# Optimization experiments

Measured on AMD Instinct MI355X. Metric: run time of the kernel, lower is better.

Reference implementation:

```python
import jax, jax.numpy as jnp
import numpy as np
import math

D_MODEL, N_HEADS, D_K, D_V = 512, 2, 64, 64
C_CLIP = 10.0
MASK_FILL = -10.0

def setup_inputs() -> dict:
    key = jax.random.key(0)
    ks = jax.random.split(key, 12)
    B, Lq, Lk = 4, 2048, 2048
    s = 1.0 / math.sqrt(D_MODEL)
    return {
        "Q": jax.random.normal(ks[0], (B, Lq, D_MODEL), jnp.float32),
        "K": jax.random.normal(ks[1], (B, Lk, D_MODEL), jnp.float32),
        "V": jax.random.normal(ks[2], (B, Lk, D_MODEL), jnp.float32),
        "mask": jax.random.randint(ks[3], (B, Lk), 0, 2) > 0,
        "Wq": jax.random.normal(ks[4], (D_MODEL, N_HEADS * D_K), jnp.float32) * s,
        "bq": jnp.zeros((N_HEADS * D_K,), jnp.float32),
        "Wk": jax.random.normal(ks[5], (D_MODEL, N_HEADS * D_K), jnp.float32) * s,
        "bk": jnp.zeros((N_HEADS * D_K,), jnp.float32),
        "Wv": jax.random.normal(ks[6], (D_MODEL, N_HEADS * D_V), jnp.float32) * s,
        "bv": jnp.zeros((N_HEADS * D_V,), jnp.float32),
        "Wo": jax.random.normal(ks[7], (N_HEADS * D_V, D_MODEL), jnp.float32) * s,
        "bo": jnp.zeros((D_MODEL,), jnp.float32),
    }

def reference(Q, K, V, mask, Wq, bq, Wk, bk, Wv, bv, Wo, bo):
    B, Lq, _ = Q.shape
    Lk = K.shape[1]
    # project and split heads: [B, h, L, d]
    q = (Q @ Wq + bq).reshape(B, Lq, N_HEADS, D_K).transpose(0, 2, 1, 3)
    k = (K @ Wk + bk).reshape(B, Lk, N_HEADS, D_K).transpose(0, 2, 1, 3)
    v = (V @ Wv + bv).reshape(B, Lk, N_HEADS, D_V).transpose(0, 2, 1, 3)
    scores = jnp.einsum("bhqd,bhkd->bhqk", q, k) / jnp.sqrt(jnp.float32(D_K))
    scores = jnp.tanh(scores) * C_CLIP
    scores = jnp.where(mask[:, None, None, :], MASK_FILL, scores)
    attn = jax.nn.log_softmax(scores, axis=-1)  # NOTE: log-softmax used directly as weights
    out = jnp.einsum("bhqk,bhkd->bhqd", attn, v)
    out = out.transpose(0, 2, 1, 3).reshape(B, Lq, N_HEADS * D_V)
    out = out @ Wo + bo
    return (out, attn)
```

## Files before the change

kernel.cpp:

```cpp
#include <hip/hip_runtime.h>

typedef __attribute__((ext_vector_type(8))) short short8;
typedef __attribute__((ext_vector_type(4))) float f32x4;

#define DEVI static __device__ __forceinline__

constexpr int NB   = 4;
constexpr int NH   = 2;
constexpr int SEQ  = 2048;
constexpr int DM   = 512;
constexpr int DKV  = 64;
constexpr int HDIM = 128;

DEVI unsigned short f2bf(float f) {
    union { float f; unsigned u; } v; v.f = f;
    unsigned r = v.u + 0x7FFFu + ((v.u >> 16) & 1u);
    return (unsigned short)(r >> 16);
}
DEVI float bf2f(unsigned short s) {
    union { unsigned u; float f; } v; v.u = ((unsigned)s) << 16; return v.f;
}
DEVI void async16(const void* g, void* l) {
    __builtin_amdgcn_global_load_lds(
        (const __attribute__((address_space(1))) unsigned int*)g,
        (__attribute__((address_space(3))) unsigned int*)l, 16, 0, 0);
}

__global__ __launch_bounds__(256) void k_prep(
    const float* __restrict__ Wq, const float* __restrict__ Wk,
    const float* __restrict__ Wv, const float* __restrict__ Wo,
    unsigned short* __restrict__ Wqt, unsigned short* __restrict__ Wkt,
    unsigned short* __restrict__ Wvt, unsigned short* __restrict__ Wot) {
    int id = blockIdx.x * 256 + threadIdx.x;
    int which = id >> 16;
    int rem = id & 65535;
    if (which < 3) {
        const float* W = which == 0 ? Wq : (which == 1 ? Wk : Wv);
        unsigned short* Wt = which == 0 ? Wqt : (which == 1 ? Wkt : Wvt);
        int n = rem >> 9, k = rem & 511;
        Wt[rem] = f2bf(W[k * HDIM + n]);
    } else {
        int n = rem >> 7, k = rem & 127;
        Wot[rem] = f2bf(Wo[k * DM + n]);
    }
}

__global__ __launch_bounds__(256) void k_proj(
    const float* __restrict__ Qg, const float* __restrict__ Kg, const float* __restrict__ Vg,
    const unsigned short* __restrict__ Wqt, const unsigned short* __restrict__ Wkt,
    const unsigned short* __restrict__ Wvt,
    const float* __restrict__ bq, const float* __restrict__ bk, const float* __restrict__ bv,
    unsigned short* __restrict__ qs, unsigned short* __restrict__ kb,
    unsigned short* __restrict__ vt) {
    __shared__ unsigned short lA[32 * 64];
    __shared__ unsigned short lB[128 * 64];

    const int y = blockIdx.y;
    const float* X = y == 0 ? Qg : (y == 1 ? Kg : Vg);
    const unsigned short* Wt = y == 0 ? Wqt : (y == 1 ? Wkt : Wvt);
    const float* bias = y == 0 ? bq : (y == 1 ? bk : bv);
    const float scal = y == 0 ? 0.25f : 1.0f;
    const int row0 = blockIdx.x * 32;
    const int tid = threadIdx.x, lane = tid & 63, wv = tid >> 6;
    const int l16 = lane & 15, lq4 = lane >> 4;
    const int wc = wv;

    f32x4 acc[2][2];
    #pragma unroll
    for (int i = 0; i < 2; ++i)
        #pragma unroll
        for (int j = 0; j < 2; ++j) acc[i][j] = f32x4{0.f, 0.f, 0.f, 0.f};

    const int arow = tid >> 3, ac0 = (tid & 7) * 8;

    for (int kc = 0; kc < 8; ++kc) {
        {
            const float* src = X + (size_t)(row0 + arow) * DM + kc * 64 + ac0;
            float4 v0 = *(const float4*)src;
            float4 v1 = *(const float4*)(src + 4);
            unsigned q0 = (unsigned)f2bf(v0.x) | ((unsigned)f2bf(v0.y) << 16);
            unsigned q1 = (unsigned)f2bf(v0.z) | ((unsigned)f2bf(v0.w) << 16);
            unsigned q2 = (unsigned)f2bf(v1.x) | ((unsigned)f2bf(v1.y) << 16);
            unsigned q3 = (unsigned)f2bf(v1.z) | ((unsigned)f2bf(v1.w) << 16);
            int slot = (tid & 7) ^ (arow & 7);
            unsigned* d = (unsigned*)((char*)lA + arow * 128 + slot * 16);
            d[0] = q0; d[1] = q1; d[2] = q2; d[3] = q3;
        }
        #pragma unroll
        for (int c = 0; c < 4; ++c) {
            int chunk = wv * 4 + c;
            int n = chunk * 8 + (lane >> 3);
            int gslot = (lane & 7) ^ (n & 7);
            const void* g = (const char*)Wt + ((size_t)n * DM + kc * 64) * 2 + gslot * 16;
            void* l = (char*)lB + chunk * 1024 + lane * 16;
            async16(g, l);
        }
        __syncthreads();

        #pragma unroll
        for (int ks = 0; ks < 2; ++ks) {
            short8 a[2], b[2];
            #pragma unroll
            for (int mt = 0; mt < 2; ++mt) {
                int m = mt * 16 + l16;
                unsigned ao = (unsigned)(m * 128 + ks * 64 + lq4 * 16) ^ ((unsigned)(m & 7) << 4);
                a[mt] = *(const short8*)((const char*)lA + ao);
            }
            #pragma unroll
            for (int nt = 0; nt < 2; ++nt) {
                int n = wc * 32 + nt * 16 + l16;
                unsigned bo2 = (unsigned)(n * 128 + ks * 64 + lq4 * 16) ^ ((unsigned)(n & 7) << 4);
                b[nt] = *(const short8*)((const char*)lB + bo2);
            }
            #pragma unroll
            for (int mt = 0; mt < 2; ++mt)
                #pragma unroll
                for (int nt = 0; nt < 2; ++nt)
                    acc[mt][nt] = __builtin_amdgcn_mfma_f32_16x16x32_bf16(
                        a[mt], b[nt], acc[mt][nt], 0, 0, 0);
        }
        __syncthreads();
    }

    if (y < 2) {
        unsigned short* dstp = (y == 0) ? qs : kb;
        #pragma unroll
        for (int mt = 0; mt < 2; ++mt)
            #pragma unroll
            for (int nt = 0; nt < 2; ++nt) {
                int col = wc * 32 + nt * 16 + l16;
                float bb = bias[col];
                int h = col >> 6, d = col & 63;
                #pragma unroll
                for (int r = 0; r < 4; ++r) {
                    int row = row0 + mt * 16 + lq4 * 4 + r;
                    int b = row >> 11, pos = row & 2047;
                    float val = (acc[mt][nt][r] + bb) * scal;
                    dstp[((size_t)(b * NH + h) * SEQ + pos) * DKV + d] = f2bf(val);
                }
            }
    } else {
        #pragma unroll
        for (int mt = 0; mt < 2; ++mt)
            #pragma unroll
            for (int nt = 0; nt < 2; ++nt) {
                int col = wc * 32 + nt * 16 + l16;
                float bb = bias[col];
                #pragma unroll
                for (int r = 0; r < 4; ++r) {
                    int mrow = mt * 16 + lq4 * 4 + r;
                    lB[col * 32 + mrow] = f2bf(acc[mt][nt][r] + bb);
                }
            }
        __syncthreads();
        int c = tid >> 1, mp = (tid & 1) * 16;
        int b = row0 >> 11, kpos0 = row0 & 2047;
        int h = c >> 6, d = c & 63;
        unsigned short* dst = vt + ((size_t)(b * NH + h) * DKV + d) * SEQ + kpos0 + mp;
        const unsigned short* srcl = &lB[c * 32 + mp];
        *(uint4*)dst = *(const uint4*)srcl;
        *(uint4*)(dst + 8) = *(const uint4*)(srcl + 8);
    }
}

__global__ __launch_bounds__(512) void k_vsum(const unsigned short* __restrict__ vt,
                                              float* __restrict__ vs) {
    int bh = blockIdx.x, tid = threadIdx.x;
    int d = tid >> 3, oct = tid & 7;
    const unsigned short* src = vt + ((size_t)bh * DKV + d) * SEQ + oct * 256;
    float s = 0.f;
    #pragma unroll 4
    for (int i = 0; i < 32; ++i) {
        short8 v = *(const short8*)(src + i * 8);
        #pragma unroll
        for (int t = 0; t < 8; ++t) s += bf2f((unsigned short)v[t]);
    }
    s += __shfl_xor(s, 1); s += __shfl_xor(s, 2); s += __shfl_xor(s, 4);
    if (oct == 0) vs[bh * DKV + d] = s;
}

__global__ __launch_bounds__(1024, 4) void k_fused(
    const unsigned short* __restrict__ qs, const unsigned short* __restrict__ kb,
    const unsigned short* __restrict__ vt, const int* __restrict__ maskg,
    const float* __restrict__ vsumG, float* __restrict__ attnG,
    unsigned short* __restrict__ outh) {
    __shared__ unsigned short sAttn[32 * 2048];
    __shared__ float lsum[8][32];
    __shared__ float lL[32];
    __shared__ float pvbuf[8][16][16];

    const int wg = blockIdx.x;
    const int swz = (wg & 7) * 64 + (wg >> 3);
    const int bh = swz >> 6;
    const int qt = swz & 63;
    const int qbase = qt * 32;
    const int b = bh >> 1, h = bh & 1;
    const int tid = threadIdx.x, lane = tid & 63, wv = tid >> 6;
    const int l16 = lane & 15, lq4 = lane >> 4;
    const int wr = wv >> 3, wc8 = wv & 7;

    const unsigned short* qrow =
        qs + ((size_t)bh * SEQ + qbase + wr * 16 + l16) * DKV + lq4 * 8;
    short8 aq0 = *(const short8*)qrow;
    short8 aq1 = *(const short8*)(qrow + 32);

    const unsigned short* kfrag =
        kb + ((size_t)bh * SEQ + wc8 * 16 + l16) * DKV + lq4 * 8;
    const int* mrow = maskg + b * SEQ + wc8 * 16 + l16;

    const int srow = wr * 16 + lq4 * 4;
    const int cb = wc8 * 16 + l16;

    float sums[4] = {0.f, 0.f, 0.f, 0.f};

    short8 b0 = *(const short8*)kfrag;
    short8 b1 = *(const short8*)(kfrag + 32);
    int mv = mrow[0];
    for (int kt = 0; kt < 16; ++kt) {
        int nx = (kt + 1) & 15;
        short8 nb0 = *(const short8*)(kfrag + (size_t)nx * 8192);
        short8 nb1 = *(const short8*)(kfrag + (size_t)nx * 8192 + 32);
        int nmv = mrow[nx * 128];
        f32x4 acc = f32x4{0.f, 0.f, 0.f, 0.f};
        acc = __builtin_amdgcn_mfma_f32_16x16x32_bf16(aq0, b0, acc, 0, 0, 0);
        acc = __builtin_amdgcn_mfma_f32_16x16x32_bf16(aq1, b1, acc, 0, 0, 0);
        int col = kt * 128 + cb;
        #pragma unroll
        for (int r = 0; r < 4; ++r) {
            float x = acc[r];
            float e2 = __expf(x);
            float s10 = 10.f - 20.f * __builtin_amdgcn_rcpf(1.f + e2);
            float s = mv ? -10.f : s10;
            sums[r] += __expf(s);
            int row = srow + r;
            unsigned bo = (unsigned)(row * 4096 + col * 2) ^ ((unsigned)(row & 7) << 4);
            *(unsigned short*)((char*)sAttn + bo) = f2bf(s);
        }
        b0 = nb0; b1 = nb1; mv = nmv;
    }

    #pragma unroll
    for (int r = 0; r < 4; ++r) {
        float v = sums[r];
        v += __shfl_xor(v, 1); v += __shfl_xor(v, 2);
        v += __shfl_xor(v, 4); v += __shfl_xor(v, 8);
        if (l16 == 0) lsum[wc8][srow + r] = v;
    }
    __syncthreads();
    if (tid < 32) {
        float t = lsum[0][tid] + lsum[1][tid] + lsum[2][tid] + lsum[3][tid] +
                  lsum[4][tid] + lsum[5][tid] + lsum[6][tid] + lsum[7][tid];
        lL[tid] = __logf(t);
    }
    __syncthreads();

    {
        const int row = tid >> 5;
        const int cb2 = (tid & 31) * 8;
        const float Lv = lL[row];
        float* gdst = attnG + ((size_t)bh * SEQ + qbase + row) * SEQ;
        const unsigned rbase = (unsigned)(row * 4096);
        const unsigned rxor = (unsigned)(row & 7) << 4;
        #pragma unroll
        for (int j = 0; j < 8; ++j) {
            int c = cb2 + j * 256;
            unsigned bo = (rbase + (unsigned)(c * 2)) ^ rxor;
            short8 v = *(const short8*)((const char*)sAttn + bo);
            float4 fa, fb;
            fa.x = bf2f((unsigned short)v[0]) - Lv;
            fa.y = bf2f((unsigned short)v[1]) - Lv;
            fa.z = bf2f((unsigned short)v[2]) - Lv;
            fa.w = bf2f((unsigned short)v[3]) - Lv;
            fb.x = bf2f((unsigned short)v[4]) - Lv;
            fb.y = bf2f((unsigned short)v[5]) - Lv;
            fb.z = bf2f((unsigned short)v[6]) - Lv;
            fb.w = bf2f((unsigned short)v[7]) - Lv;
            *(float4*)(gdst + c) = fa;
            *(float4*)(gdst + c + 4) = fb;
        }
    }

    const int kh = wv >> 3, dg = (wv >> 1) & 3, pr = wv & 1;
    const unsigned short* vfrag =
        vt + ((size_t)bh * DKV + dg * 16 + l16) * SEQ + kh * 1024 + lq4 * 8;
    const int arow = pr * 16 + l16;
    const unsigned abase = (unsigned)(arow * 4096 + kh * 2048 + lq4 * 16);
    const unsigned axor = (unsigned)(arow & 7) << 4;
    f32x4 o = f32x4{0.f, 0.f, 0.f, 0.f};
    short8 vf = *(const short8*)vfrag;
    for (int ks = 0; ks < 32; ++ks) {
        short8 nvf = *(const short8*)(vfrag + ((ks + 1) & 31) * 32);
        short8 af = *(const short8*)((const char*)sAttn +
                                     ((abase + (unsigned)(ks * 64)) ^ axor));
        o = __builtin_amdgcn_mfma_f32_16x16x32_bf16(af, vf, o, 0, 0, 0);
        vf = nvf;
    }
    if (kh) {
        #pragma unroll
        for (int r = 0; r < 4; ++r) pvbuf[dg * 2 + pr][lq4 * 4 + r][l16] = o[r];
    }
    __syncthreads();
    if (!kh) {
        const float vs = vsumG[bh * DKV + dg * 16 + l16];
        #pragma unroll
        for (int r = 0; r < 4; ++r) {
            int qr = pr * 16 + lq4 * 4 + r;
            float val = o[r] + pvbuf[dg * 2 + pr][lq4 * 4 + r][l16] - lL[qr] * vs;
            outh[((size_t)b * SEQ + qbase + qr) * HDIM + h * DKV + dg * 16 + l16] =
                f2bf(val);
        }
    }
}

__global__ __launch_bounds__(256) void k_oproj(
    const unsigned short* __restrict__ outh, const unsigned short* __restrict__ Wot,
    const float* __restrict__ bo, float* __restrict__ outG) {
    __shared__ unsigned short lA2[128 * 128];
    __shared__ unsigned short lB2[128 * 128];
    const int row0 = blockIdx.x * 128, col0 = blockIdx.y * 128;
    const int tid = threadIdx.x, lane = tid & 63, wv = tid >> 6;
    const int l16 = lane & 15, lq4 = lane >> 4;
    const int wr = wv >> 1, wc = wv & 1;

    #pragma unroll
    for (int c = 0; c < 8; ++c) {
        int chunk = wv * 8 + c;
        int row = chunk * 4 + (lane >> 4);
        int gslot = (lane & 15) ^ (row & 7);
        async16((const char*)outh + ((size_t)(row0 + row)) * 256 + gslot * 16,
                (char*)lA2 + chunk * 1024 + lane * 16);
    }
    #pragma unroll
    for (int c = 0; c < 8; ++c) {
        int chunk = wv * 8 + c;
        int row = chunk * 4 + (lane >> 4);
        int gslot = (lane & 15) ^ (row & 7);
        async16((const char*)Wot + ((size_t)(col0 + row)) * 256 + gslot * 16,
                (char*)lB2 + chunk * 1024 + lane * 16);
    }
    __syncthreads();

    f32x4 acc[4][4];
    #pragma unroll
    for (int mt = 0; mt < 4; ++mt)
        #pragma unroll
        for (int nt = 0; nt < 4; ++nt) acc[mt][nt] = f32x4{0.f, 0.f, 0.f, 0.f};

    #pragma unroll
    for (int ks = 0; ks < 4; ++ks) {
        short8 a[4], bfr[4];
        #pragma unroll
        for (int mt = 0; mt < 4; ++mt) {
            int m = wr * 64 + mt * 16 + l16;
            unsigned ao = (unsigned)(m * 256 + ks * 64 + lq4 * 16) ^ ((unsigned)(m & 7) << 4);
            a[mt] = *(const short8*)((const char*)lA2 + ao);
        }
        #pragma unroll
        for (int nt = 0; nt < 4; ++nt) {
            int n = wc * 64 + nt * 16 + l16;
            unsigned bo2 = (unsigned)(n * 256 + ks * 64 + lq4 * 16) ^ ((unsigned)(n & 7) << 4);
            bfr[nt] = *(const short8*)((const char*)lB2 + bo2);
        }
        #pragma unroll
        for (int mt = 0; mt < 4; ++mt)
            #pragma unroll
            for (int nt = 0; nt < 4; ++nt)
                acc[mt][nt] = __builtin_amdgcn_mfma_f32_16x16x32_bf16(
                    a[mt], bfr[nt], acc[mt][nt], 0, 0, 0);
    }

    #pragma unroll
    for (int nt = 0; nt < 4; ++nt) {
        int col = col0 + wc * 64 + nt * 16 + l16;
        float bb = bo[col];
        #pragma unroll
        for (int mt = 0; mt < 4; ++mt)
            #pragma unroll
            for (int r = 0; r < 4; ++r) {
                int row = row0 + wr * 64 + mt * 16 + lq4 * 4 + r;
                outG[(size_t)row * DM + col] = acc[mt][nt][r] + bb;
            }
    }
}

extern "C" void kernel_launch(void* const* d_in, const int* in_sizes, int n_in,
                              void* d_out, int out_size, void* d_ws, size_t ws_size,
                              hipStream_t stream) {
    (void)in_sizes; (void)n_in; (void)out_size; (void)ws_size;
    const float* Qg = (const float*)d_in[0];
    const float* Kg = (const float*)d_in[1];
    const float* Vg = (const float*)d_in[2];
    const int*   maskg = (const int*)d_in[3];
    const float* Wq = (const float*)d_in[4];
    const float* bq = (const float*)d_in[5];
    const float* Wk = (const float*)d_in[6];
    const float* bk = (const float*)d_in[7];
    const float* Wv = (const float*)d_in[8];
    const float* bv = (const float*)d_in[9];
    const float* Wo = (const float*)d_in[10];
    const float* bo = (const float*)d_in[11];

    char* ws = (char*)d_ws;
    unsigned short* qs   = (unsigned short*)(ws);
    unsigned short* kb   = (unsigned short*)(ws + (4  << 20));
    unsigned short* vt   = (unsigned short*)(ws + (8  << 20));
    unsigned short* outh = (unsigned short*)(ws + (28 << 20));
    float*          vsum = (float*)(ws + (30 << 20));
    unsigned short* Wqt  = (unsigned short*)(ws + (30 << 20) + 262144);
    unsigned short* Wkt  = (unsigned short*)((char*)Wqt + 131072);
    unsigned short* Wvt  = (unsigned short*)((char*)Wkt + 131072);
    unsigned short* Wot  = (unsigned short*)((char*)Wvt + 131072);

    float* outG  = (float*)d_out;
    float* attnG = outG + (size_t)NB * SEQ * DM;

    hipLaunchKernelGGL(k_prep, dim3(1024), dim3(256), 0, stream,
                       Wq, Wk, Wv, Wo, Wqt, Wkt, Wvt, Wot);
    hipLaunchKernelGGL(k_proj, dim3(256, 3), dim3(256), 0, stream,
                       Qg, Kg, Vg, Wqt, Wkt, Wvt, bq, bk, bv, qs, kb, vt);
    hipLaunchKernelGGL(k_vsum, dim3(8), dim3(512), 0, stream, vt, vsum);
    hipLaunchKernelGGL(k_fused, dim3(512), dim3(1024), 0, stream,
                       qs, kb, vt, maskg, vsum, attnG, outh);
    hipLaunchKernelGGL(k_oproj, dim3(64, 4), dim3(256), 0, stream, outh, Wot, bo, outG);
}
```

Measured before the change: 283.7 us.

## Split fused attention into QK and PV kernels; double-buffer projection GEMM

The fused attention kernel, which held a 32x2048 score tile in LDS, is split into two kernels. k_qk computes clipped, masked scores for 16-row tiles, writes bf16 scores and the per-row log-sum-exp to a global workspace. k_pvfin then reads them back to compute the PV product and write the fp32 log-softmax output. Separately, the projection GEMM gets double-buffered LDS with register prefetch of the next X chunk, overlapping loads with MFMA. The split aims to cut LDS use and raise occupancy, at the cost of a 64MB bf16 score round-trip through global memory.

```diff
diff --git a/kernel.cpp b/kernel.cpp
--- a/kernel.cpp
+++ b/kernel.cpp
@@ -19,6 +19,9 @@
 }
 DEVI float bf2f(unsigned short s) {
     union { unsigned u; float f; } v; v.u = ((unsigned)s) << 16; return v.f;
+}
+DEVI unsigned pk2(float a, float b) {
+    return (unsigned)f2bf(a) | ((unsigned)f2bf(b) << 16);
 }
 DEVI void async16(const void* g, void* l) {
     __builtin_amdgcn_global_load_lds(
@@ -52,8 +55,8 @@
     const float* __restrict__ bq, const float* __restrict__ bk, const float* __restrict__ bv,
     unsigned short* __restrict__ qs, unsigned short* __restrict__ kb,
     unsigned short* __restrict__ vt) {
-    __shared__ unsigned short lA[32 * 64];
-    __shared__ unsigned short lB[128 * 64];
+    __shared__ unsigned short lA[2][32 * 64];
+    __shared__ unsigned short lB[2][128 * 64];
 
     const int y = blockIdx.y;
     const float* X = y == 0 ? Qg : (y == 1 ? Kg : Vg);
@@ -72,31 +75,42 @@
         for (int j = 0; j < 2; ++j) acc[i][j] = f32x4{0.f, 0.f, 0.f, 0.f};
 
     const int arow = tid >> 3, ac0 = (tid & 7) * 8;
-
-    for (int kc = 0; kc < 8; ++kc) {
-        {
-            const float* src = X + (size_t)(row0 + arow) * DM + kc * 64 + ac0;
-            float4 v0 = *(const float4*)src;
-            float4 v1 = *(const float4*)(src + 4);
-            unsigned q0 = (unsigned)f2bf(v0.x) | ((unsigned)f2bf(v0.y) << 16);
-            unsigned q1 = (unsigned)f2bf(v0.z) | ((unsigned)f2bf(v0.w) << 16);
-            unsigned q2 = (unsigned)f2bf(v1.x) | ((unsigned)f2bf(v1.y) << 16);
-            unsigned q3 = (unsigned)f2bf(v1.z) | ((unsigned)f2bf(v1.w) << 16);
-            int slot = (tid & 7) ^ (arow & 7);
-            unsigned* d = (unsigned*)((char*)lA + arow * 128 + slot * 16);
-            d[0] = q0; d[1] = q1; d[2] = q2; d[3] = q3;
-        }
+    const int aslot = (tid & 7) ^ (arow & 7);
+    const float* xsrc = X + (size_t)(row0 + arow) * DM + ac0;
+
+    float4 x0 = *(const float4*)xsrc;
+    float4 x1 = *(const float4*)(xsrc + 4);
+    {
         #pragma unroll
         for (int c = 0; c < 4; ++c) {
             int chunk = wv * 4 + c;
             int n = chunk * 8 + (lane >> 3);
             int gslot = (lane & 7) ^ (n & 7);
-            const void* g = (const char*)Wt + ((size_t)n * DM + kc * 64) * 2 + gslot * 16;
-            void* l = (char*)lB + chunk * 1024 + lane * 16;
-            async16(g, l);
-        }
-        __syncthreads();
-
+            async16((const char*)Wt + ((size_t)n * DM) * 2 + gslot * 16,
+                    (char*)lB[0] + chunk * 1024 + lane * 16);
+        }
+    }
+    float4 y0 = *(const float4*)(xsrc + 64);
+    float4 y1 = *(const float4*)(xsrc + 68);
+    {
+        unsigned* d = (unsigned*)((char*)lA[0] + arow * 128 + aslot * 16);
+        d[0] = pk2(x0.x, x0.y); d[1] = pk2(x0.z, x0.w);
+        d[2] = pk2(x1.x, x1.y); d[3] = pk2(x1.z, x1.w);
+    }
+    __syncthreads();
+
+    for (int kc = 0; kc < 8; ++kc) {
+        const int cur = kc & 1, nxt = cur ^ 1;
+        if (kc < 7) {
+            #pragma unroll
+            for (int c = 0; c < 4; ++c) {
+                int chunk = wv * 4 + c;
+                int n = chunk * 8 + (lane >> 3);
+                int gslot = (lane & 7) ^ (n & 7);
+                async16((const char*)Wt + ((size_t)n * DM + (kc + 1) * 64) * 2 + gslot * 16,
+                        (char*)lB[nxt] + chunk * 1024 + lane * 16);
+            }
+        }
         #pragma unroll
         for (int ks = 0; ks < 2; ++ks) {
             short8 a[2], b[2];
@@ -104,13 +118,13 @@
             for (int mt = 0; mt < 2; ++mt) {
                 int m = mt * 16 + l16;
                 unsigned ao = (unsigned)(m * 128 + ks * 64 + lq4 * 16) ^ ((unsigned)(m & 7) << 4);
-                a[mt] = *(const short8*)((const char*)lA + ao);
+                a[mt] = *(const short8*)((const char*)lA[cur] + ao);
             }
             #pragma unroll
             for (int nt = 0; nt < 2; ++nt) {
                 int n = wc * 32 + nt * 16 + l16;
                 unsigned bo2 = (unsigned)(n * 128 + ks * 64 + lq4 * 16) ^ ((unsigned)(n & 7) << 4);
-                b[nt] = *(const short8*)((const char*)lB + bo2);
+                b[nt] = *(const short8*)((const char*)lB[cur] + bo2);
             }
             #pragma unroll
             for (int mt = 0; mt < 2; ++mt)
@@ -118,6 +132,15 @@
                 for (int nt = 0; nt < 2; ++nt)
                     acc[mt][nt] = __builtin_amdgcn_mfma_f32_16x16x32_bf16(
                         a[mt], b[nt], acc[mt][nt], 0, 0, 0);
+        }
+        if (kc < 7) {
+            unsigned* d = (unsigned*)((char*)lA[nxt] + arow * 128 + aslot * 16);
+            d[0] = pk2(y0.x, y0.y); d[1] = pk2(y0.z, y0.w);
+            d[2] = pk2(y1.x, y1.y); d[3] = pk2(y1.z, y1.w);
+            if (kc < 6) {
+                y0 = *(const float4*)(xsrc + (kc + 2) * 64);
+                y1 = *(const float4*)(xsrc + (kc + 2) * 64 + 4);
+            }
         }
         __syncthreads();
     }
@@ -149,7 +172,7 @@
                 #pragma unroll
                 for (int r = 0; r < 4; ++r) {
                     int mrow = mt * 16 + lq4 * 4 + r;
-                    lB[col * 32 + mrow] = f2bf(acc[mt][nt][r] + bb);
+                    lB[0][col * 32 + mrow] = f2bf(acc[mt][nt][r] + bb);
                 }
             }
         __syncthreads();
@@ -157,7 +180,7 @@
         int b = row0 >> 11, kpos0 = row0 & 2047;
         int h = c >> 6, d = c & 63;
         unsigned short* dst = vt + ((size_t)(b * NH + h) * DKV + d) * SEQ + kpos0 + mp;
-        const unsigned short* srcl = &lB[c * 32 + mp];
+        const unsigned short* srcl = &lB[0][c * 32 + mp];
         *(uint4*)dst = *(const uint4*)srcl;
         *(uint4*)(dst + 8) = *(const uint4*)(srcl + 8);
     }
@@ -179,52 +202,44 @@
     if (oct == 0) vs[bh * DKV + d] = s;
 }
 
-__global__ __launch_bounds__(1024, 4) void k_fused(
+__global__ __launch_bounds__(512, 4) void k_qk(
     const unsigned short* __restrict__ qs, const unsigned short* __restrict__ kb,
-    const unsigned short* __restrict__ vt, const int* __restrict__ maskg,
-    const float* __restrict__ vsumG, float* __restrict__ attnG,
-    unsigned short* __restrict__ outh) {
-    __shared__ unsigned short sAttn[32 * 2048];
-    __shared__ float lsum[8][32];
-    __shared__ float lL[32];
-    __shared__ float pvbuf[8][16][16];
+    const int* __restrict__ maskg, unsigned short* __restrict__ sg,
+    float* __restrict__ Lg) {
+    __shared__ unsigned short sS[16 * 2048];
+    __shared__ float lsum[8][16];
 
     const int wg = blockIdx.x;
-    const int swz = (wg & 7) * 64 + (wg >> 3);
-    const int bh = swz >> 6;
-    const int qt = swz & 63;
-    const int qbase = qt * 32;
-    const int b = bh >> 1, h = bh & 1;
+    const int bh = wg & 7;
+    const int qt = wg >> 3;
+    const int qbase = qt * 16;
+    const int b = bh >> 1;
     const int tid = threadIdx.x, lane = tid & 63, wv = tid >> 6;
     const int l16 = lane & 15, lq4 = lane >> 4;
-    const int wr = wv >> 3, wc8 = wv & 7;
 
     const unsigned short* qrow =
-        qs + ((size_t)bh * SEQ + qbase + wr * 16 + l16) * DKV + lq4 * 8;
+        qs + ((size_t)bh * SEQ + qbase + l16) * DKV + lq4 * 8;
     short8 aq0 = *(const short8*)qrow;
     short8 aq1 = *(const short8*)(qrow + 32);
 
-    const unsigned short* kfrag =
-        kb + ((size_t)bh * SEQ + wc8 * 16 + l16) * DKV + lq4 * 8;
-    const int* mrow = maskg + b * SEQ + wc8 * 16 + l16;
-
-    const int srow = wr * 16 + lq4 * 4;
-    const int cb = wc8 * 16 + l16;
+    const unsigned short* kf =
+        kb + ((size_t)bh * SEQ + wv * 256 + l16) * DKV + lq4 * 8;
+    const int* mrow = maskg + b * SEQ + wv * 256 + l16;
 
     float sums[4] = {0.f, 0.f, 0.f, 0.f};
 
-    short8 b0 = *(const short8*)kfrag;
-    short8 b1 = *(const short8*)(kfrag + 32);
+    short8 b0 = *(const short8*)kf;
+    short8 b1 = *(const short8*)(kf + 32);
     int mv = mrow[0];
     for (int kt = 0; kt < 16; ++kt) {
         int nx = (kt + 1) & 15;
-        short8 nb0 = *(const short8*)(kfrag + (size_t)nx * 8192);
-        short8 nb1 = *(const short8*)(kfrag + (size_t)nx * 8192 + 32);
-        int nmv = mrow[nx * 128];
+        short8 nb0 = *(const short8*)(kf + nx * 1024);
+        short8 nb1 = *(const short8*)(kf + nx * 1024 + 32);
+        int nmv = mrow[nx * 16];
         f32x4 acc = f32x4{0.f, 0.f, 0.f, 0.f};
         acc = __builtin_amdgcn_mfma_f32_16x16x32_bf16(aq0, b0, acc, 0, 0, 0);
         acc = __builtin_amdgcn_mfma_f32_16x16x32_bf16(aq1, b1, acc, 0, 0, 0);
-        int col = kt * 128 + cb;
+        int col = wv * 256 + kt * 16 + l16;
         #pragma unroll
         for (int r = 0; r < 4; ++r) {
             float x = acc[r];
@@ -232,9 +247,9 @@
             float s10 = 10.f - 20.f * __builtin_amdgcn_rcpf(1.f + e2);
             float s = mv ? -10.f : s10;
             sums[r] += __expf(s);
-            int row = srow + r;
+            int row = lq4 * 4 + r;
             unsigned bo = (unsigned)(row * 4096 + col * 2) ^ ((unsigned)(row & 7) << 4);
-            *(unsigned short*)((char*)sAttn + bo) = f2bf(s);
+            *(unsigned short*)((char*)sS + bo) = f2bf(s);
         }
         b0 = nb0; b1 = nb1; mv = nmv;
     }
@@ -244,28 +259,77 @@
         float v = sums[r];
         v += __shfl_xor(v, 1); v += __shfl_xor(v, 2);
         v += __shfl_xor(v, 4); v += __shfl_xor(v, 8);
-        if (l16 == 0) lsum[wc8][srow + r] = v;
+        if (l16 == 0) lsum[wv][lq4 * 4 + r] = v;
     }
     __syncthreads();
-    if (tid < 32) {
+
+    if (tid < 16) {
         float t = lsum[0][tid] + lsum[1][tid] + lsum[2][tid] + lsum[3][tid] +
                   lsum[4][tid] + lsum[5][tid] + lsum[6][tid] + lsum[7][tid];
-        lL[tid] = __logf(t);
-    }
-    __syncthreads();
+        Lg[(size_t)bh * SEQ + qbase + tid] = __logf(t);
+    }
 
     {
-        const int row = tid >> 5;
-        const int cb2 = (tid & 31) * 8;
-        const float Lv = lL[row];
+        const int row = tid >> 5, t32 = tid & 31;
+        unsigned short* gdst = sg + ((size_t)bh * SEQ + qbase + row) * SEQ;
+        const unsigned rxor = (unsigned)(row & 7) << 4;
+        const unsigned rbase = (unsigned)(row * 4096);
+        #pragma unroll
+        for (int j = 0; j < 8; ++j) {
+            unsigned off = (unsigned)(t32 * 16 + j * 512);
+            short8 v = *(const short8*)((const char*)sS + ((rbase + off) ^ rxor));
+            *(short8*)((char*)gdst + off) = v;
+        }
+    }
+}
+
+__global__ __launch_bounds__(256, 4) void k_pvfin(
+    const unsigned short* __restrict__ sg, const unsigned short* __restrict__ vt,
+    const float* __restrict__ Lg, const float* __restrict__ vsumG,
+    float* __restrict__ attnG, unsigned short* __restrict__ outh) {
+    const int wg = blockIdx.x;
+    const int bh = wg & 7;
+    const int qt = wg >> 3;
+    const int qbase = qt * 16;
+    const int b = bh >> 1, h = bh & 1;
+    const int tid = threadIdx.x, lane = tid & 63, dg = tid >> 6;
+    const int l16 = lane & 15, lq4 = lane >> 4;
+
+    const unsigned short* aptr =
+        sg + ((size_t)bh * SEQ + qbase + l16) * SEQ + lq4 * 8;
+    const unsigned short* vptr =
+        vt + ((size_t)bh * DKV + dg * 16 + l16) * SEQ + lq4 * 8;
+
+    f32x4 o = f32x4{0.f, 0.f, 0.f, 0.f};
+    short8 af = *(const short8*)aptr;
+    short8 vf = *(const short8*)vptr;
+    for (int ks = 0; ks < 64; ++ks) {
+        int nk = (ks + 1) & 63;
+        short8 naf = *(const short8*)(aptr + nk * 32);
+        short8 nvf = *(const short8*)(vptr + nk * 32);
+        o = __builtin_amdgcn_mfma_f32_16x16x32_bf16(af, vf, o, 0, 0, 0);
+        af = naf; vf = nvf;
+    }
+    {
+        const float vs = vsumG[bh * DKV + dg * 16 + l16];
+        #pragma unroll
+        for (int r = 0; r < 4; ++r) {
+            int qr = qbase + lq4 * 4 + r;
+            float Lv = Lg[(size_t)bh * SEQ + qr];
+            float val = o[r] - Lv * vs;
+            outh[((size_t)b * SEQ + qr) * HDIM + h * DKV + dg * 16 + l16] = f2bf(val);
+        }
+    }
+
+    {
+        const int row = tid >> 4, seg = tid & 15;
+        const unsigned short* srow = sg + ((size_t)bh * SEQ + qbase + row) * SEQ;
+        const float Lv = Lg[(size_t)bh * SEQ + qbase + row];
         float* gdst = attnG + ((size_t)bh * SEQ + qbase + row) * SEQ;
-        const unsigned rbase = (unsigned)(row * 4096);
-        const unsigned rxor = (unsigned)(row & 7) << 4;
-        #pragma unroll
-        for (int j = 0; j < 8; ++j) {
-            int c = cb2 + j * 256;
-            unsigned bo = (rbase + (unsigned)(c * 2)) ^ rxor;
-            short8 v = *(const short8*)((const char*)sAttn + bo);
+        #pragma unroll
+        for (int j = 0; j < 16; ++j) {
+            int c = j * 128 + seg * 8;
+            short8 v = *(const short8*)(srow + c);
             float4 fa, fb;
             fa.x = bf2f((unsigned short)v[0]) - Lv;
             fa.y = bf2f((unsigned short)v[1]) - Lv;
@@ -277,37 +341,6 @@
             fb.w = bf2f((unsigned short)v[7]) - Lv;
             *(float4*)(gdst + c) = fa;
             *(float4*)(gdst + c + 4) = fb;
-        }
-    }
-
-    const int kh = wv >> 3, dg = (wv >> 1) & 3, pr = wv & 1;
-    const unsigned short* vfrag =
-        vt + ((size_t)bh * DKV + dg * 16 + l16) * SEQ + kh * 1024 + lq4 * 8;
-    const int arow = pr * 16 + l16;
-    const unsigned abase = (unsigned)(arow * 4096 + kh * 2048 + lq4 * 16);
-    const unsigned axor = (unsigned)(arow & 7) << 4;
-    f32x4 o = f32x4{0.f, 0.f, 0.f, 0.f};
-    short8 vf = *(const short8*)vfrag;
-    for (int ks = 0; ks < 32; ++ks) {
-        short8 nvf = *(const short8*)(vfrag + ((ks + 1) & 31) * 32);
-        short8 af = *(const short8*)((const char*)sAttn +
-                                     ((abase + (unsigned)(ks * 64)) ^ axor));
-        o = __builtin_amdgcn_mfma_f32_16x16x32_bf16(af, vf, o, 0, 0, 0);
-        vf = nvf;
-    }
-    if (kh) {
-        #pragma unroll
-        for (int r = 0; r < 4; ++r) pvbuf[dg * 2 + pr][lq4 * 4 + r][l16] = o[r];
-    }
-    __syncthreads();
-    if (!kh) {
-        const float vs = vsumG[bh * DKV + dg * 16 + l16];
-        #pragma unroll
-        for (int r = 0; r < 4; ++r) {
-            int qr = pr * 16 + lq4 * 4 + r;
-            float val = o[r] + pvbuf[dg * 2 + pr][lq4 * 4 + r][l16] - lL[qr] * vs;
-            outh[((size_t)b * SEQ + qbase + qr) * HDIM + h * DKV + dg * 16 + l16] =
-                f2bf(val);
         }
     }
 }
@@ -410,6 +443,8 @@
     unsigned short* Wkt  = (unsigned short*)((char*)Wqt + 131072);
     unsigned short* Wvt  = (unsigned short*)((char*)Wkt + 131072);
     unsigned short* Wot  = (unsigned short*)((char*)Wvt + 131072);
+    unsigned short* sg   = (unsigned short*)(ws + ((size_t)32 << 20));
+    float*          Lg   = (float*)(ws + ((size_t)96 << 20));
 
     float* outG  = (float*)d_out;
     float* attnG = outG + (size_t)NB * SEQ * DM;
@@ -419,7 +454,9 @@
     hipLaunchKernelGGL(k_proj, dim3(256, 3), dim3(256), 0, stream,
                        Qg, Kg, Vg, Wqt, Wkt, Wvt, bq, bk, bv, qs, kb, vt);
     hipLaunchKernelGGL(k_vsum, dim3(8), dim3(512), 0, stream, vt, vsum);
-    hipLaunchKernelGGL(k_fused, dim3(512), dim3(1024), 0, stream,
-                       qs, kb, vt, maskg, vsum, attnG, outh);
+    hipLaunchKernelGGL(k_qk, dim3(1024), dim3(512), 0, stream,
+                       qs, kb, maskg, sg, Lg);
+    hipLaunchKernelGGL(k_pvfin, dim3(1024), dim3(256), 0, stream,
+                       sg, vt, Lg, vsum, attnG, outh);
     hipLaunchKernelGGL(k_oproj, dim3(64, 4), dim3(256), 0, stream, outh, Wot, bo, outG);
 }
```

Result: slower. 327.9 us (+15.6%).
